# Kernel tuning notes

Hardware: AMD Instinct MI355X
Metric: run time of the kernel (lower is better)

Reference implementation:

```python
import jax, jax.numpy as jnp
import numpy as np

EPS = 1e-5

def _layernorm(x, gamma, beta):
    mu = jnp.mean(x, axis=-1, keepdims=True)
    var = jnp.var(x, axis=-1, keepdims=True)
    return (x - mu) * jax.lax.rsqrt(var + EPS) * gamma + beta

def setup_inputs() -> dict:
    key = jax.random.key(0)
    ks = jax.random.split(key, 6)
    bs, t, dim = 4, 2048, 1024
    x = jax.random.normal(ks[0], (bs, t, dim), dtype=jnp.float32)
    # shared LayerNorm params (same module applied twice in forward)
    ln_gamma = jnp.ones((dim,), dtype=jnp.float32)
    ln_beta = jnp.zeros((dim,), dtype=jnp.float32)
    # Linear params, stored as (in, out)
    w1 = jax.random.normal(ks[1], (dim, 2 * dim), dtype=jnp.float32) / np.sqrt(dim)
    b1 = jax.random.normal(ks[2], (2 * dim,), dtype=jnp.float32) * 0.01
    w2 = jax.random.normal(ks[3], (2 * dim, dim), dtype=jnp.float32) / np.sqrt(2 * dim)
    b2 = jax.random.normal(ks[4], (dim,), dtype=jnp.float32) * 0.01
    return {"x": x, "ln_gamma": ln_gamma, "ln_beta": ln_beta,
            "w1": w1, "b1": b1, "w2": w2, "b2": b2}

def reference(x, ln_gamma, ln_beta, w1, b1, w2, b2):
    # x: [bs, t, f]
    y = _layernorm(x, ln_gamma, ln_beta)
    y = jax.nn.gelu(jnp.einsum('btf,fh->bth', y, w1) + b1, approximate=False)
    y = jnp.einsum('bth,hf->btf', y, w2) + b2
    # attention-like quadratic mix (no softmax): (x @ x^T) @ y
    scores = jnp.einsum('btf,bsf->bts', x, x)          # [bs, t, t]
    y = jnp.einsum('bts,bsf->btf', scores, y)
    y = x + y
    y = _layernorm(y, ln_gamma, ln_beta)
    return y
```

## Files before the change

### kernel.cpp

```cpp
#include <hip/hip_runtime.h>
#include <hip/hip_fp16.h>

typedef _Float16 f16;
typedef _Float16 f16x8 __attribute__((ext_vector_type(8)));
typedef _Float16 f16x4 __attribute__((ext_vector_type(4)));
typedef float f32x4 __attribute__((ext_vector_type(4)));

#define LN_EPS 1e-5f

__device__ __forceinline__ float erf_fast(float x) {
    const float ax = __builtin_fabsf(x);
    const float t = 1.0f / (1.0f + 0.3275911f * ax);
    const float y = t * (0.254829592f +
                    t * (-0.284496736f +
                    t * (1.421413741f +
                    t * (-1.453152027f +
                    t * 1.061405429f))));
    const float r = 1.0f - y * __expf(-ax * ax);
    return __builtin_copysignf(r, x);
}

__device__ __forceinline__ float gelu_exact(float v) {
    return 0.5f * v * (1.0f + erf_fast(v * 0.70710678118654752440f));
}

__device__ __forceinline__ void gload_lds16(const f16* g, f16* l) {
    __builtin_amdgcn_global_load_lds(
        (const __attribute__((address_space(1))) unsigned int*)(g),
        (__attribute__((address_space(3))) unsigned int*)(l),
        16, 0, 0);
}

__global__ __launch_bounds__(256)
void ln_cast_kernel(const float* __restrict__ x,
                    const float* __restrict__ gamma,
                    const float* __restrict__ beta,
                    f16* __restrict__ y_h,
                    f16* __restrict__ x_h) {
    const int row = blockIdx.x;
    const int t = threadIdx.x;
    const size_t base = (size_t)row * 1024;
    float4 v = ((const float4*)(x + base))[t];
    float s  = v.x + v.y + v.z + v.w;
    float s2 = v.x*v.x + v.y*v.y + v.z*v.z + v.w*v.w;
    #pragma unroll
    for (int off = 32; off > 0; off >>= 1) {
        s  += __shfl_down(s, off, 64);
        s2 += __shfl_down(s2, off, 64);
    }
    __shared__ float ls[4], ls2[4];
    const int wid = t >> 6;
    if ((t & 63) == 0) { ls[wid] = s; ls2[wid] = s2; }
    __syncthreads();
    if (t == 0) {
        ls[0]  = ls[0] + ls[1] + ls[2] + ls[3];
        ls2[0] = ls2[0] + ls2[1] + ls2[2] + ls2[3];
    }
    __syncthreads();
    const float mu   = ls[0] * (1.0f / 1024.0f);
    const float var  = ls2[0] * (1.0f / 1024.0f) - mu * mu;
    const float rstd = rsqrtf(var + LN_EPS);
    const float4 g  = ((const float4*)gamma)[t];
    const float4 bt = ((const float4*)beta)[t];
    f16x4 yo, xo;
    yo[0] = (f16)((v.x - mu) * rstd * g.x + bt.x);
    yo[1] = (f16)((v.y - mu) * rstd * g.y + bt.y);
    yo[2] = (f16)((v.z - mu) * rstd * g.z + bt.z);
    yo[3] = (f16)((v.w - mu) * rstd * g.w + bt.w);
    xo[0] = (f16)v.x; xo[1] = (f16)v.y; xo[2] = (f16)v.z; xo[3] = (f16)v.w;
    *(f16x4*)(y_h + base + t * 4) = yo;
    *(f16x4*)(x_h + base + t * 4) = xo;
}

__global__ __launch_bounds__(256)
void ln_final_kernel(const float* __restrict__ pre,
                     const float* __restrict__ gamma,
                     const float* __restrict__ beta,
                     float* __restrict__ out) {
    const int row = blockIdx.x;
    const int t = threadIdx.x;
    const size_t base = (size_t)row * 1024;
    float4 v = ((const float4*)(pre + base))[t];
    float s  = v.x + v.y + v.z + v.w;
    float s2 = v.x*v.x + v.y*v.y + v.z*v.z + v.w*v.w;
    #pragma unroll
    for (int off = 32; off > 0; off >>= 1) {
        s  += __shfl_down(s, off, 64);
        s2 += __shfl_down(s2, off, 64);
    }
    __shared__ float ls[4], ls2[4];
    const int wid = t >> 6;
    if ((t & 63) == 0) { ls[wid] = s; ls2[wid] = s2; }
    __syncthreads();
    if (t == 0) {
        ls[0]  = ls[0] + ls[1] + ls[2] + ls[3];
        ls2[0] = ls2[0] + ls2[1] + ls2[2] + ls2[3];
    }
    __syncthreads();
    const float mu   = ls[0] * (1.0f / 1024.0f);
    const float var  = ls2[0] * (1.0f / 1024.0f) - mu * mu;
    const float rstd = rsqrtf(var + LN_EPS);
    const float4 g  = ((const float4*)gamma)[t];
    const float4 bt = ((const float4*)beta)[t];
    float4 o;
    o.x = (v.x - mu) * rstd * g.x + bt.x;
    o.y = (v.y - mu) * rstd * g.y + bt.y;
    o.z = (v.z - mu) * rstd * g.z + bt.z;
    o.w = (v.w - mu) * rstd * g.w + bt.w;
    ((float4*)(out + base))[t] = o;
}

__global__ __launch_bounds__(256)
void transpose_cast_kernel(const float* __restrict__ src,
                           f16* __restrict__ dst, int R, int C) {
    __shared__ float tile[32][33];
    const int c0 = blockIdx.x * 32, r0 = blockIdx.y * 32;
    const int tx = threadIdx.x & 31, ty = threadIdx.x >> 5;
    #pragma unroll
    for (int i = 0; i < 4; ++i) {
        const int r = ty + i * 8;
        tile[r][tx] = src[(size_t)(r0 + r) * C + c0 + tx];
    }
    __syncthreads();
    #pragma unroll
    for (int i = 0; i < 4; ++i) {
        const int r = ty + i * 8;
        dst[(size_t)(c0 + r) * R + r0 + tx] = (f16)tile[tx][r];
    }
}

__global__ __launch_bounds__(256)
void transpose_f16_kernel(const f16* __restrict__ src,
                          f16* __restrict__ dst, int R, int C) {
    __shared__ f16 tile[32][33];
    const size_t zb = (size_t)blockIdx.z * R * C;
    src += zb; dst += zb;
    const int c0 = blockIdx.x * 32, r0 = blockIdx.y * 32;
    const int tx = threadIdx.x & 31, ty = threadIdx.x >> 5;
    #pragma unroll
    for (int i = 0; i < 4; ++i) {
        const int r = ty + i * 8;
        tile[r][tx] = src[(size_t)(r0 + r) * C + c0 + tx];
    }
    __syncthreads();
    #pragma unroll
    for (int i = 0; i < 4; ++i) {
        const int r = ty + i * 8;
        dst[(size_t)(c0 + r) * R + r0 + tx] = tile[tx][r];
    }
}

template <int EPI>
__global__ __launch_bounds__(512, 2)
void gemm256_nt_kernel(const f16* __restrict__ A, const f16* __restrict__ Bt,
                       const float* __restrict__ bias, f16* __restrict__ outH,
                       int M, int N, int K) {
    __shared__ __attribute__((aligned(16))) f16 sAbuf[2][256 * 64];
    __shared__ __attribute__((aligned(16))) f16 sBbuf[2][256 * 64];

    const int m0 = blockIdx.x * 256;
    const int n0 = blockIdx.y * 256;
    const int t = threadIdx.x;
    const int l = t & 63;
    const int wid = t >> 6;
    const int wr = wid >> 2;
    const int wc = wid & 3;
    const int rl = l & 15;
    const int g  = l >> 4;
    const int nk = K >> 6;

    const int rowS = wid * 16 + (l >> 3);
    const int kbS  = ((l & 7) ^ ((l >> 3) & 7)) * 8;
    const f16* pA = A  + (size_t)(m0 + rowS) * K + kbS;
    const f16* pB = Bt + (size_t)(n0 + rowS) * K + kbS;
    const int ldsS = wid * 1024;

    const int rA = wr * 128 + rl;
    const int rB = wc * 64 + rl;
    const int swk0 = ((g)     ^ (rl & 7)) * 8;
    const int swk1 = ((4 + g) ^ (rl & 7)) * 8;

    f32x4 acc[8][4] = {};

    const long long hstep = (long long)128 * K;

    auto stgA = [&](f16* dst, int h, int kc) {
        const f16* s = pA + (size_t)h * hstep + kc * 64;
        f16* d = dst + h * 8192 + ldsS;
        gload_lds16(s, d);
        gload_lds16(s + 8 * K, d + 512);
    };
    auto stgB = [&](f16* dst, int h, int kc) {
        const f16* s = pB + (size_t)h * hstep + kc * 64;
        f16* d = dst + h * 8192 + ldsS;
        gload_lds16(s, d);
        gload_lds16(s + 8 * K, d + 512);
    };

    f16* bufA0 = sAbuf[0]; f16* bufA1 = sAbuf[1];
    f16* bufB0 = sBbuf[0]; f16* bufB1 = sBbuf[1];

    const int t1 = (nk > 1) ? 1 : 0;
    stgA(bufA0, 0, 0); stgA(bufA0, 1, 0);
    stgB(bufB0, 0, 0); stgB(bufB0, 1, 0);
    stgB(bufB1, 0, t1); stgB(bufB1, 1, t1);
    stgA(bufA1, 0, t1);
    asm volatile("s_waitcnt vmcnt(6)" ::: "memory");
    __builtin_amdgcn_s_barrier();

    f16 *Ac = bufA0, *Ao = bufA1, *Bc = bufB0, *Bo = bufB1;

    f16x8 a[4][2], b0r[2][2], b1r[2][2];

    for (int kt = 0; kt < nk; ++kt) {
        const int kt1 = (kt + 1 < nk) ? kt + 1 : nk - 1;
        const int kt2 = (kt + 2 < nk) ? kt + 2 : nk - 1;

        #pragma unroll
        for (int fm = 0; fm < 4; ++fm) {
            a[fm][0] = *(const f16x8*)(Ac + (rA + fm * 16) * 64 + swk0);
            a[fm][1] = *(const f16x8*)(Ac + (rA + fm * 16) * 64 + swk1);
        }
        #pragma unroll
        for (int fn = 0; fn < 2; ++fn) {
            b0r[fn][0] = *(const f16x8*)(Bc + (rB + fn * 16) * 64 + swk0);
            b0r[fn][1] = *(const f16x8*)(Bc + (rB + fn * 16) * 64 + swk1);
        }
        stgA(Ao, 1, kt1);
        __builtin_amdgcn_s_barrier();
        asm volatile("s_waitcnt lgkmcnt(0)" ::: "memory");
        __builtin_amdgcn_sched_barrier(0);
        __builtin_amdgcn_s_setprio(1);
        #pragma unroll
        for (int fm = 0; fm < 4; ++fm)
            #pragma unroll
            for (int fn = 0; fn < 2; ++fn) {
                acc[fm][fn] = __builtin_amdgcn_mfma_f32_16x16x32_f16(a[fm][0], b0r[fn][0], acc[fm][fn], 0, 0, 0);
                acc[fm][fn] = __builtin_amdgcn_mfma_f32_16x16x32_f16(a[fm][1], b0r[fn][1], acc[fm][fn], 0, 0, 0);
            }
        __builtin_amdgcn_s_setprio(0);
        __builtin_amdgcn_s_barrier();

        #pragma unroll
        for (int fn = 0; fn < 2; ++fn) {
            b1r[fn][0] = *(const f16x8*)(Bc + (rB + (fn + 2) * 16) * 64 + swk0);
            b1r[fn][1] = *(const f16x8*)(Bc + (rB + (fn + 2) * 16) * 64 + swk1);
        }
        __builtin_amdgcn_s_barrier();
        asm volatile("s_waitcnt lgkmcnt(0)" ::: "memory");
        __builtin_amdgcn_sched_barrier(0);
        __builtin_amdgcn_s_setprio(1);
        #pragma unroll
        for (int fm = 0; fm < 4; ++fm)
            #pragma unroll
            for (int fn = 0; fn < 2; ++fn) {
                acc[fm][fn + 2] = __builtin_amdgcn_mfma_f32_16x16x32_f16(a[fm][0], b1r[fn][0], acc[fm][fn + 2], 0, 0, 0);
                acc[fm][fn + 2] = __builtin_amdgcn_mfma_f32_16x16x32_f16(a[fm][1], b1r[fn][1], acc[fm][fn + 2], 0, 0, 0);
            }
        __builtin_amdgcn_s_setprio(0);
        __builtin_amdgcn_s_barrier();

        #pragma unroll
        for (int fm = 0; fm < 4; ++fm) {
            a[fm][0] = *(const f16x8*)(Ac + (rA + (fm + 4) * 16) * 64 + swk0);
            a[fm][1] = *(const f16x8*)(Ac + (rA + (fm + 4) * 16) * 64 + swk1);
        }
        stgB(Bc, 0, kt2);
        __builtin_amdgcn_s_barrier();
        asm volatile("s_waitcnt lgkmcnt(0)" ::: "memory");
        __builtin_amdgcn_sched_barrier(0);
        __builtin_amdgcn_s_setprio(1);
        #pragma unroll
        for (int fm = 0; fm < 4; ++fm)
            #pragma unroll
            for (int fn = 0; fn < 2; ++fn) {
                acc[fm + 4][fn + 2] = __builtin_amdgcn_mfma_f32_16x16x32_f16(a[fm][0], b1r[fn][0], acc[fm + 4][fn + 2], 0, 0, 0);
                acc[fm + 4][fn + 2] = __builtin_amdgcn_mfma_f32_16x16x32_f16(a[fm][1], b1r[fn][1], acc[fm + 4][fn + 2], 0, 0, 0);
            }
        __builtin_amdgcn_s_setprio(0);
        __builtin_amdgcn_s_barrier();

        stgB(Bc, 1, kt2);
        stgA(Ac, 0, kt2);
        __builtin_amdgcn_s_barrier();
        __builtin_amdgcn_s_setprio(1);
        #pragma unroll
        for (int fm = 0; fm < 4; ++fm)
            #pragma unroll
            for (int fn = 0; fn < 2; ++fn) {
                acc[fm + 4][fn] = __builtin_amdgcn_mfma_f32_16x16x32_f16(a[fm][0], b0r[fn][0], acc[fm + 4][fn], 0, 0, 0);
                acc[fm + 4][fn] = __builtin_amdgcn_mfma_f32_16x16x32_f16(a[fm][1], b0r[fn][1], acc[fm + 4][fn], 0, 0, 0);
            }
        __builtin_amdgcn_s_setprio(0);
        asm volatile("s_waitcnt vmcnt(6)" ::: "memory");
        __builtin_amdgcn_s_barrier();

        f16* tp;
        tp = Ac; Ac = Ao; Ao = tp;
        tp = Bc; Bc = Bo; Bo = tp;
    }
    asm volatile("s_waitcnt vmcnt(0)" ::: "memory");

    #pragma unroll
    for (int fm = 0; fm < 8; ++fm) {
        #pragma unroll
        for (int fn = 0; fn < 4; ++fn) {
            const int col = n0 + wc * 64 + fn * 16 + rl;
            const float bv = bias[col];
            #pragma unroll
            for (int r = 0; r < 4; ++r) {
                const int row = m0 + wr * 128 + fm * 16 + g * 4 + r;
                const float v = acc[fm][fn][r] + bv;
                outH[(size_t)row * N + col] = (f16)gelu_exact(v);
            }
        }
    }
}

template <int EPI>
__global__ __launch_bounds__(512, 2)
void gemm256x128_nt_kernel(const f16* __restrict__ A, const f16* __restrict__ Bt,
                           const float* __restrict__ bias,
                           const float* __restrict__ xadd,
                           f16* __restrict__ outH, float* __restrict__ outF,
                           int M, int N, int K,
                           long long batchA, long long batchB, long long batchC) {
    __shared__ __attribute__((aligned(16))) f16 sA[3][256 * 64];
    __shared__ __attribute__((aligned(16))) f16 sB[3][128 * 64];

    const int z = blockIdx.z;
    A  += (size_t)z * batchA;
    Bt += (size_t)z * batchB;

    const int m0 = blockIdx.x * 256;
    const int n0 = blockIdx.y * 128;
    const int t = threadIdx.x;
    const int l = t & 63;
    const int wid = t >> 6;
    const int wr = wid >> 1;
    const int wc = wid & 1;
    const int rl = l & 15;
    const int g  = l >> 4;
    const int nk = K >> 6;

    const int rowS = t >> 3;
    const int kbS  = ((t & 7) ^ (rowS & 7)) * 8;
    const f16* pA = A  + (size_t)(m0 + rowS) * K + kbS;
    const f16* pB = Bt + (size_t)(n0 + rowS) * K + kbS;
    const int ldsS = wid * 512;

    const int rA = wr * 64 + rl;
    const int rB = wc * 64 + rl;
    const int swk0 = ((g)     ^ (rl & 7)) * 8;
    const int swk1 = ((4 + g) ^ (rl & 7)) * 8;

    f32x4 acc[4][4] = {};

    auto stgA = [&](f16* dst, int u, int kc) {
        gload_lds16(pA + (size_t)u * 64 * K + kc * 64, dst + u * 4096 + ldsS);
    };
    auto stgB = [&](f16* dst, int u, int kc) {
        gload_lds16(pB + (size_t)u * 64 * K + kc * 64, dst + u * 4096 + ldsS);
    };

    const int t1 = (nk > 1) ? 1 : 0;
    #pragma unroll
    for (int u = 0; u < 4; ++u) stgA(sA[0], u, 0);
    #pragma unroll
    for (int u = 0; u < 2; ++u) stgB(sB[0], u, 0);
    #pragma unroll
    for (int u = 0; u < 4; ++u) stgA(sA[1], u, t1);
    #pragma unroll
    for (int u = 0; u < 2; ++u) stgB(sB[1], u, t1);

    f16 *curA = sA[0], *nxtA = sA[1], *farA = sA[2];
    f16 *curB = sB[0], *nxtB = sB[1], *farB = sB[2];

    f16x8 a[4][2], b[4][2];

    for (int kt = 0; kt < nk; ++kt) {
        asm volatile("s_waitcnt vmcnt(6)" ::: "memory");
        __builtin_amdgcn_s_barrier();

        const int kt2 = (kt + 2 < nk) ? kt + 2 : nk - 1;

        #pragma unroll
        for (int fm = 0; fm < 2; ++fm) {
            a[fm][0] = *(const f16x8*)(curA + (rA + fm * 16) * 64 + swk0);
            a[fm][1] = *(const f16x8*)(curA + (rA + fm * 16) * 64 + swk1);
        }
        #pragma unroll
        for (int fn = 0; fn < 2; ++fn) {
            b[fn][0] = *(const f16x8*)(curB + (rB + fn * 16) * 64 + swk0);
            b[fn][1] = *(const f16x8*)(curB + (rB + fn * 16) * 64 + swk1);
        }
        stgA(farA, 0, kt2);
        stgA(farA, 1, kt2);
        asm volatile("s_waitcnt lgkmcnt(0)" ::: "memory");
        __builtin_amdgcn_sched_barrier(0);
        __builtin_amdgcn_s_setprio(1);
        #pragma unroll
        for (int fm = 0; fm < 2; ++fm)
            #pragma unroll
            for (int fn = 0; fn < 2; ++fn) {
                acc[fm][fn] = __builtin_amdgcn_mfma_f32_16x16x32_f16(a[fm][0], b[fn][0], acc[fm][fn], 0, 0, 0);
                acc[fm][fn] = __builtin_amdgcn_mfma_f32_16x16x32_f16(a[fm][1], b[fn][1], acc[fm][fn], 0, 0, 0);
            }
        __builtin_amdgcn_s_setprio(0);

        #pragma unroll
        for (int fn = 2; fn < 4; ++fn) {
            b[fn][0] = *(const f16x8*)(curB + (rB + fn * 16) * 64 + swk0);
            b[fn][1] = *(const f16x8*)(curB + (rB + fn * 16) * 64 + swk1);
        }
        stgA(farA, 2, kt2);
        stgA(farA, 3, kt2);
        asm volatile("s_waitcnt lgkmcnt(0)" ::: "memory");
        __builtin_amdgcn_sched_barrier(0);
        __builtin_amdgcn_s_setprio(1);
        #pragma unroll
        for (int fm = 0; fm < 2; ++fm)
            #pragma unroll
            for (int fn = 2; fn < 4; ++fn) {
                acc[fm][fn] = __builtin_amdgcn_mfma_f32_16x16x32_f16(a[fm][0], b[fn][0], acc[fm][fn], 0, 0, 0);
                acc[fm][fn] = __builtin_amdgcn_mfma_f32_16x16x32_f16(a[fm][1], b[fn][1], acc[fm][fn], 0, 0, 0);
            }
        __builtin_amdgcn_s_setprio(0);

        #pragma unroll
        for (int fm = 2; fm < 4; ++fm) {
            a[fm][0] = *(const f16x8*)(curA + (rA + fm * 16) * 64 + swk0);
            a[fm][1] = *(const f16x8*)(curA + (rA + fm * 16) * 64 + swk1);
        }
        stgB(farB, 0, kt2);
        stgB(farB, 1, kt2);
        asm volatile("s_waitcnt lgkmcnt(0)" ::: "memory");
        __builtin_amdgcn_sched_barrier(0);
        __builtin_amdgcn_s_setprio(1);
        #pragma unroll
        for (int fm = 2; fm < 4; ++fm)
            #pragma unroll
            for (int fn = 2; fn < 4; ++fn) {
                acc[fm][fn] = __builtin_amdgcn_mfma_f32_16x16x32_f16(a[fm][0], b[fn][0], acc[fm][fn], 0, 0, 0);
                acc[fm][fn] = __builtin_amdgcn_mfma_f32_16x16x32_f16(a[fm][1], b[fn][1], acc[fm][fn], 0, 0, 0);
            }
        __builtin_amdgcn_s_setprio(0);

        __builtin_amdgcn_s_setprio(1);
        #pragma unroll
        for (int fm = 2; fm < 4; ++fm)
            #pragma unroll
            for (int fn = 0; fn < 2; ++fn) {
                acc[fm][fn] = __builtin_amdgcn_mfma_f32_16x16x32_f16(a[fm][0], b[fn][0], acc[fm][fn], 0, 0, 0);
                acc[fm][fn] = __builtin_amdgcn_mfma_f32_16x16x32_f16(a[fm][1], b[fn][1], acc[fm][fn], 0, 0, 0);
            }
        __builtin_amdgcn_s_setprio(0);

        f16* tp;
        tp = curA; curA = nxtA; nxtA = farA; farA = tp;
        tp = curB; curB = nxtB; nxtB = farB; farB = tp;
    }
    asm volatile("s_waitcnt vmcnt(0)" ::: "memory");

    const float* xaddz = xadd;
    float* outFz = outF;
    if (EPI == 3) {
        outFz += (size_t)z * batchC;
        xaddz += (size_t)z * batchC;
    }
    #pragma unroll
    for (int fm = 0; fm < 4; ++fm) {
        #pragma unroll
        for (int fn = 0; fn < 4; ++fn) {
            const int col = n0 + wc * 64 + fn * 16 + rl;
            if (EPI == 1) {
                const int row0 = m0 + wr * 64 + fm * 16 + g * 4;
                const int zz = row0 >> 11;
                const int rr = row0 & 2047;
                const float bv = bias[col];
                f16x4 o;
                #pragma unroll
                for (int r = 0; r < 4; ++r) o[r] = (f16)(acc[fm][fn][r] + bv);
                *(f16x4*)(outH + ((size_t)zz * N + col) * 2048 + rr) = o;
            } else {
                #pragma unroll
                for (int r = 0; r < 4; ++r) {
                    const int row = m0 + wr * 64 + fm * 16 + g * 4 + r;
                    const size_t idx = (size_t)row * N + col;
                    outFz[idx] = acc[fm][fn][r] + xaddz[idx];
                }
            }
        }
    }
}

template <int EPI>
__global__ __launch_bounds__(256, 3)
void gemm_nt_kernel(const f16* __restrict__ A, const f16* __restrict__ Bt,
                    f16* __restrict__ outH,
                    int M, int N, int K,
                    long long batchA, long long batchB, long long batchC) {
    __shared__ __attribute__((aligned(16))) f16 sA[3][128 * 32];
    __shared__ __attribute__((aligned(16))) f16 sB[3][128 * 32];

    const int z = blockIdx.z;
    A  += (size_t)z * batchA;
    Bt += (size_t)z * batchB;

    const int m0 = blockIdx.x * 128;
    const int n0 = blockIdx.y * 128;
    const int t = threadIdx.x;
    const int l = t & 63;
    const int wid = t >> 6;
    const int wm = (wid >> 1) * 64;
    const int wn = (wid & 1) * 64;

    f32x4 acc[4][4] = {};

    const int rl = l & 15;
    const int nk = K >> 5;

    const int row0 = t >> 2;
    const int kb = ((t & 3) ^ (row0 & 3)) * 8;
    const f16* Ag0 = A  + (size_t)(m0 + row0) * K + kb;
    const f16* Ag1 = A  + (size_t)(m0 + row0 + 64) * K + kb;
    const f16* Bg0 = Bt + (size_t)(n0 + row0) * K + kb;
    const f16* Bg1 = Bt + (size_t)(n0 + row0 + 64) * K + kb;
    const int lo0 = wid * 512;
    const int lo1 = 2048 + wid * 512;

    const int swk = (((l >> 4) ^ (rl & 3))) * 8;

    gload_lds16(Ag0,      sA[0] + lo0);
    gload_lds16(Ag1,      sA[0] + lo1);
    gload_lds16(Bg0,      sB[0] + lo0);
    gload_lds16(Bg1,      sB[0] + lo1);
    gload_lds16(Ag0 + 32, sA[1] + lo0);
    gload_lds16(Ag1 + 32, sA[1] + lo1);
    gload_lds16(Bg0 + 32, sB[1] + lo0);
    gload_lds16(Bg1 + 32, sB[1] + lo1);

    f16 *curA = sA[0], *nxtA = sA[1], *farA = sA[2];
    f16 *curB = sB[0], *nxtB = sB[1], *farB = sB[2];

    for (int kt = 0; kt < nk; ++kt) {
        asm volatile("s_waitcnt vmcnt(4)" ::: "memory");
        __builtin_amdgcn_s_barrier();

        const int ktn = (kt + 2 < nk) ? kt + 2 : nk - 1;
        const int kof = ktn * 32;
        gload_lds16(Ag0 + kof, farA + lo0);
        gload_lds16(Ag1 + kof, farA + lo1);
        gload_lds16(Bg0 + kof, farB + lo0);
        gload_lds16(Bg1 + kof, farB + lo1);

        f16x8 a[4], b[4];
        #pragma unroll
        for (int f = 0; f < 4; ++f) {
            a[f] = *(const f16x8*)&curA[(wm + f * 16 + rl) * 32 + swk];
            b[f] = *(const f16x8*)&curB[(wn + f * 16 + rl) * 32 + swk];
        }
        #pragma unroll
        for (int fm = 0; fm < 4; ++fm)
            #pragma unroll
            for (int fn = 0; fn < 4; ++fn)
                acc[fm][fn] = __builtin_amdgcn_mfma_f32_16x16x32_f16(
                    a[fm], b[fn], acc[fm][fn], 0, 0, 0);

        f16* tA = curA; curA = nxtA; nxtA = farA; farA = tA;
        f16* tB = curB; curB = nxtB; nxtB = farB; farB = tB;
    }
    asm volatile("s_waitcnt vmcnt(0)" ::: "memory");

    const int rh = l >> 4;
    f16* outHz = outH + (size_t)z * batchC;
    #pragma unroll
    for (int fm = 0; fm < 4; ++fm) {
        #pragma unroll
        for (int fn = 0; fn < 4; ++fn) {
            const int col = n0 + wn + fn * 16 + rl;
            #pragma unroll
            for (int r = 0; r < 4; ++r) {
                const int row = m0 + wm + fm * 16 + rh * 4 + r;
                outHz[(size_t)row * N + col] = (f16)acc[fm][fn][r];
            }
        }
    }
}

extern "C" void kernel_launch(void* const* d_in, const int* in_sizes, int n_in,
                              void* d_out, int out_size, void* d_ws, size_t ws_size,
                              hipStream_t stream) {
    const float* x     = (const float*)d_in[0];
    const float* gamma = (const float*)d_in[1];
    const float* beta  = (const float*)d_in[2];
    const float* w1    = (const float*)d_in[3];
    const float* b1    = (const float*)d_in[4];
    const float* w2    = (const float*)d_in[5];
    const float* b2    = (const float*)d_in[6];
    float* out = (float*)d_out;

    const int BS = 4, T = 2048, DIM = 1024, HID = 2048;
    const int M = BS * T;
    const long long MB = 1024 * 1024;

    char* ws = (char*)d_ws;
    f16*   x_h  = (f16*)(ws + 0 * MB);
    f16*   y_h  = (f16*)(ws + 16 * MB);
    f16*   h    = (f16*)(ws + 32 * MB);
    float* pre  = (float*)h;
    f16*   y2t  = (f16*)(ws + 64 * MB);
    f16*   x_t  = (f16*)(ws + 80 * MB);
    f16*   G    = (f16*)(ws + 96 * MB);
    f16*   w1t  = (f16*)(ws + 104 * MB);
    f16*   w2t  = (f16*)(ws + 108 * MB);

    ln_cast_kernel<<<M, 256, 0, stream>>>(x, gamma, beta, y_h, x_h);

    transpose_cast_kernel<<<dim3(HID / 32, DIM / 32), 256, 0, stream>>>(w1, w1t, DIM, HID);
    transpose_cast_kernel<<<dim3(DIM / 32, HID / 32), 256, 0, stream>>>(w2, w2t, HID, DIM);

    gemm256_nt_kernel<0><<<dim3(M / 256, HID / 256), 512, 0, stream>>>(
        y_h, w1t, b1, h, M, HID, DIM);

    gemm256x128_nt_kernel<1><<<dim3(M / 256, DIM / 128, 1), 512, 0, stream>>>(
        h, w2t, b2, nullptr, y2t, nullptr, M, DIM, HID, 0, 0, 0);

    transpose_f16_kernel<<<dim3(DIM / 32, T / 32, BS), 256, 0, stream>>>(x_h, x_t, T, DIM);

    gemm_nt_kernel<2><<<dim3(DIM / 128, DIM / 128, BS), 256, 0, stream>>>(
        y2t, x_t, G, DIM, DIM, T,
        (long long)DIM * T, (long long)DIM * T, (long long)DIM * DIM);

    gemm256x128_nt_kernel<3><<<dim3(T / 256, DIM / 128, BS), 512, 0, stream>>>(
        x_h, G, nullptr, x, nullptr, pre, T, DIM, DIM,
        (long long)T * DIM, (long long)DIM * DIM, (long long)T * DIM);

    ln_final_kernel<<<M, 256, 0, stream>>>(pre, gamma, beta, out);
}
```

Baseline: 198.4 us.

## Swap MFMA operands for row-contiguous vector stores; reuse 256x128 kernel for first GEMM

Swaps the A/B operands of the MFMA instructions in most GEMM epilogues, so each lane holds four consecutive columns of one row. This lets the epilogues write f16x4 or float4 vectors instead of scattered scalar stores, and read bias and the residual as float4. The 256x256 first-GEMM kernel is removed, and the first GEMM now runs on the 256x128 kernel with a GELU epilogue, doubling its grid. The trade is less operand reuse per block on that first GEMM in exchange for wider, coalesced stores.

```diff
diff --git a/kernel.cpp b/kernel.cpp
--- a/kernel.cpp
+++ b/kernel.cpp
@@ -152,173 +152,6 @@
 
 template <int EPI>
 __global__ __launch_bounds__(512, 2)
-void gemm256_nt_kernel(const f16* __restrict__ A, const f16* __restrict__ Bt,
-                       const float* __restrict__ bias, f16* __restrict__ outH,
-                       int M, int N, int K) {
-    __shared__ __attribute__((aligned(16))) f16 sAbuf[2][256 * 64];
-    __shared__ __attribute__((aligned(16))) f16 sBbuf[2][256 * 64];
-
-    const int m0 = blockIdx.x * 256;
-    const int n0 = blockIdx.y * 256;
-    const int t = threadIdx.x;
-    const int l = t & 63;
-    const int wid = t >> 6;
-    const int wr = wid >> 2;
-    const int wc = wid & 3;
-    const int rl = l & 15;
-    const int g  = l >> 4;
-    const int nk = K >> 6;
-
-    const int rowS = wid * 16 + (l >> 3);
-    const int kbS  = ((l & 7) ^ ((l >> 3) & 7)) * 8;
-    const f16* pA = A  + (size_t)(m0 + rowS) * K + kbS;
-    const f16* pB = Bt + (size_t)(n0 + rowS) * K + kbS;
-    const int ldsS = wid * 1024;
-
-    const int rA = wr * 128 + rl;
-    const int rB = wc * 64 + rl;
-    const int swk0 = ((g)     ^ (rl & 7)) * 8;
-    const int swk1 = ((4 + g) ^ (rl & 7)) * 8;
-
-    f32x4 acc[8][4] = {};
-
-    const long long hstep = (long long)128 * K;
-
-    auto stgA = [&](f16* dst, int h, int kc) {
-        const f16* s = pA + (size_t)h * hstep + kc * 64;
-        f16* d = dst + h * 8192 + ldsS;
-        gload_lds16(s, d);
-        gload_lds16(s + 8 * K, d + 512);
-    };
-    auto stgB = [&](f16* dst, int h, int kc) {
-        const f16* s = pB + (size_t)h * hstep + kc * 64;
-        f16* d = dst + h * 8192 + ldsS;
-        gload_lds16(s, d);
-        gload_lds16(s + 8 * K, d + 512);
-    };
-
-    f16* bufA0 = sAbuf[0]; f16* bufA1 = sAbuf[1];
-    f16* bufB0 = sBbuf[0]; f16* bufB1 = sBbuf[1];
-
-    const int t1 = (nk > 1) ? 1 : 0;
-    stgA(bufA0, 0, 0); stgA(bufA0, 1, 0);
-    stgB(bufB0, 0, 0); stgB(bufB0, 1, 0);
-    stgB(bufB1, 0, t1); stgB(bufB1, 1, t1);
-    stgA(bufA1, 0, t1);
-    asm volatile("s_waitcnt vmcnt(6)" ::: "memory");
-    __builtin_amdgcn_s_barrier();
-
-    f16 *Ac = bufA0, *Ao = bufA1, *Bc = bufB0, *Bo = bufB1;
-
-    f16x8 a[4][2], b0r[2][2], b1r[2][2];
-
-    for (int kt = 0; kt < nk; ++kt) {
-        const int kt1 = (kt + 1 < nk) ? kt + 1 : nk - 1;
-        const int kt2 = (kt + 2 < nk) ? kt + 2 : nk - 1;
-
-        #pragma unroll
-        for (int fm = 0; fm < 4; ++fm) {
-            a[fm][0] = *(const f16x8*)(Ac + (rA + fm * 16) * 64 + swk0);
-            a[fm][1] = *(const f16x8*)(Ac + (rA + fm * 16) * 64 + swk1);
-        }
-        #pragma unroll
-        for (int fn = 0; fn < 2; ++fn) {
-            b0r[fn][0] = *(const f16x8*)(Bc + (rB + fn * 16) * 64 + swk0);
-            b0r[fn][1] = *(const f16x8*)(Bc + (rB + fn * 16) * 64 + swk1);
-        }
-        stgA(Ao, 1, kt1);
-        __builtin_amdgcn_s_barrier();
-        asm volatile("s_waitcnt lgkmcnt(0)" ::: "memory");
-        __builtin_amdgcn_sched_barrier(0);
-        __builtin_amdgcn_s_setprio(1);
-        #pragma unroll
-        for (int fm = 0; fm < 4; ++fm)
-            #pragma unroll
-            for (int fn = 0; fn < 2; ++fn) {
-                acc[fm][fn] = __builtin_amdgcn_mfma_f32_16x16x32_f16(a[fm][0], b0r[fn][0], acc[fm][fn], 0, 0, 0);
-                acc[fm][fn] = __builtin_amdgcn_mfma_f32_16x16x32_f16(a[fm][1], b0r[fn][1], acc[fm][fn], 0, 0, 0);
-            }
-        __builtin_amdgcn_s_setprio(0);
-        __builtin_amdgcn_s_barrier();
-
-        #pragma unroll
-        for (int fn = 0; fn < 2; ++fn) {
-            b1r[fn][0] = *(const f16x8*)(Bc + (rB + (fn + 2) * 16) * 64 + swk0);
-            b1r[fn][1] = *(const f16x8*)(Bc + (rB + (fn + 2) * 16) * 64 + swk1);
-        }
-        __builtin_amdgcn_s_barrier();
-        asm volatile("s_waitcnt lgkmcnt(0)" ::: "memory");
-        __builtin_amdgcn_sched_barrier(0);
-        __builtin_amdgcn_s_setprio(1);
-        #pragma unroll
-        for (int fm = 0; fm < 4; ++fm)
-            #pragma unroll
-            for (int fn = 0; fn < 2; ++fn) {
-                acc[fm][fn + 2] = __builtin_amdgcn_mfma_f32_16x16x32_f16(a[fm][0], b1r[fn][0], acc[fm][fn + 2], 0, 0, 0);
-                acc[fm][fn + 2] = __builtin_amdgcn_mfma_f32_16x16x32_f16(a[fm][1], b1r[fn][1], acc[fm][fn + 2], 0, 0, 0);
-            }
-        __builtin_amdgcn_s_setprio(0);
-        __builtin_amdgcn_s_barrier();
-
-        #pragma unroll
-        for (int fm = 0; fm < 4; ++fm) {
-            a[fm][0] = *(const f16x8*)(Ac + (rA + (fm + 4) * 16) * 64 + swk0);
-            a[fm][1] = *(const f16x8*)(Ac + (rA + (fm + 4) * 16) * 64 + swk1);
-        }
-        stgB(Bc, 0, kt2);
-        __builtin_amdgcn_s_barrier();
-        asm volatile("s_waitcnt lgkmcnt(0)" ::: "memory");
-        __builtin_amdgcn_sched_barrier(0);
-        __builtin_amdgcn_s_setprio(1);
-        #pragma unroll
-        for (int fm = 0; fm < 4; ++fm)
-            #pragma unroll
-            for (int fn = 0; fn < 2; ++fn) {
-                acc[fm + 4][fn + 2] = __builtin_amdgcn_mfma_f32_16x16x32_f16(a[fm][0], b1r[fn][0], acc[fm + 4][fn + 2], 0, 0, 0);
-                acc[fm + 4][fn + 2] = __builtin_amdgcn_mfma_f32_16x16x32_f16(a[fm][1], b1r[fn][1], acc[fm + 4][fn + 2], 0, 0, 0);
-            }
-        __builtin_amdgcn_s_setprio(0);
-        __builtin_amdgcn_s_barrier();
-
-        stgB(Bc, 1, kt2);
-        stgA(Ac, 0, kt2);
-        __builtin_amdgcn_s_barrier();
-        __builtin_amdgcn_s_setprio(1);
-        #pragma unroll
-        for (int fm = 0; fm < 4; ++fm)
-            #pragma unroll
-            for (int fn = 0; fn < 2; ++fn) {
-                acc[fm + 4][fn] = __builtin_amdgcn_mfma_f32_16x16x32_f16(a[fm][0], b0r[fn][0], acc[fm + 4][fn], 0, 0, 0);
-                acc[fm + 4][fn] = __builtin_amdgcn_mfma_f32_16x16x32_f16(a[fm][1], b0r[fn][1], acc[fm + 4][fn], 0, 0, 0);
-            }
-        __builtin_amdgcn_s_setprio(0);
-        asm volatile("s_waitcnt vmcnt(6)" ::: "memory");
-        __builtin_amdgcn_s_barrier();
-
-        f16* tp;
-        tp = Ac; Ac = Ao; Ao = tp;
-        tp = Bc; Bc = Bo; Bo = tp;
-    }
-    asm volatile("s_waitcnt vmcnt(0)" ::: "memory");
-
-    #pragma unroll
-    for (int fm = 0; fm < 8; ++fm) {
-        #pragma unroll
-        for (int fn = 0; fn < 4; ++fn) {
-            const int col = n0 + wc * 64 + fn * 16 + rl;
-            const float bv = bias[col];
-            #pragma unroll
-            for (int r = 0; r < 4; ++r) {
-                const int row = m0 + wr * 128 + fm * 16 + g * 4 + r;
-                const float v = acc[fm][fn][r] + bv;
-                outH[(size_t)row * N + col] = (f16)gelu_exact(v);
-            }
-        }
-    }
-}
-
-template <int EPI>
-__global__ __launch_bounds__(512, 2)
 void gemm256x128_nt_kernel(const f16* __restrict__ A, const f16* __restrict__ Bt,
                            const float* __restrict__ bias,
                            const float* __restrict__ xadd,
@@ -356,6 +189,13 @@
 
     f32x4 acc[4][4] = {};
 
+    auto mf = [&](f32x4 c, f16x8 af, f16x8 bf) {
+        if constexpr (EPI != 1)
+            return __builtin_amdgcn_mfma_f32_16x16x32_f16(bf, af, c, 0, 0, 0);
+        else
+            return __builtin_amdgcn_mfma_f32_16x16x32_f16(af, bf, c, 0, 0, 0);
+    };
+
     auto stgA = [&](f16* dst, int u, int kc) {
         gload_lds16(pA + (size_t)u * 64 * K + kc * 64, dst + u * 4096 + ldsS);
     };
@@ -403,8 +243,8 @@
         for (int fm = 0; fm < 2; ++fm)
             #pragma unroll
             for (int fn = 0; fn < 2; ++fn) {
-                acc[fm][fn] = __builtin_amdgcn_mfma_f32_16x16x32_f16(a[fm][0], b[fn][0], acc[fm][fn], 0, 0, 0);
-                acc[fm][fn] = __builtin_amdgcn_mfma_f32_16x16x32_f16(a[fm][1], b[fn][1], acc[fm][fn], 0, 0, 0);
+                acc[fm][fn] = mf(acc[fm][fn], a[fm][0], b[fn][0]);
+                acc[fm][fn] = mf(acc[fm][fn], a[fm][1], b[fn][1]);
             }
         __builtin_amdgcn_s_setprio(0);
 
@@ -422,8 +262,8 @@
         for (int fm = 0; fm < 2; ++fm)
             #pragma unroll
             for (int fn = 2; fn < 4; ++fn) {
-                acc[fm][fn] = __builtin_amdgcn_mfma_f32_16x16x32_f16(a[fm][0], b[fn][0], acc[fm][fn], 0, 0, 0);
-                acc[fm][fn] = __builtin_amdgcn_mfma_f32_16x16x32_f16(a[fm][1], b[fn][1], acc[fm][fn], 0, 0, 0);
+                acc[fm][fn] = mf(acc[fm][fn], a[fm][0], b[fn][0]);
+                acc[fm][fn] = mf(acc[fm][fn], a[fm][1], b[fn][1]);
             }
         __builtin_amdgcn_s_setprio(0);
 
@@ -441,8 +281,8 @@
         for (int fm = 2; fm < 4; ++fm)
             #pragma unroll
             for (int fn = 2; fn < 4; ++fn) {
-                acc[fm][fn] = __builtin_amdgcn_mfma_f32_16x16x32_f16(a[fm][0], b[fn][0], acc[fm][fn], 0, 0, 0);
-                acc[fm][fn] = __builtin_amdgcn_mfma_f32_16x16x32_f16(a[fm][1], b[fn][1], acc[fm][fn], 0, 0, 0);
+                acc[fm][fn] = mf(acc[fm][fn], a[fm][0], b[fn][0]);
+                acc[fm][fn] = mf(acc[fm][fn], a[fm][1], b[fn][1]);
             }
         __builtin_amdgcn_s_setprio(0);
 
@@ -451,8 +291,8 @@
         for (int fm = 2; fm < 4; ++fm)
             #pragma unroll
             for (int fn = 0; fn < 2; ++fn) {
-                acc[fm][fn] = __builtin_amdgcn_mfma_f32_16x16x32_f16(a[fm][0], b[fn][0], acc[fm][fn], 0, 0, 0);
-                acc[fm][fn] = __builtin_amdgcn_mfma_f32_16x16x32_f16(a[fm][1], b[fn][1], acc[fm][fn], 0, 0, 0);
+                acc[fm][fn] = mf(acc[fm][fn], a[fm][0], b[fn][0]);
+                acc[fm][fn] = mf(acc[fm][fn], a[fm][1], b[fn][1]);
             }
         __builtin_amdgcn_s_setprio(0);
 
@@ -462,18 +302,12 @@
     }
     asm volatile("s_waitcnt vmcnt(0)" ::: "memory");
 
-    const float* xaddz = xadd;
-    float* outFz = outF;
-    if (EPI == 3) {
-        outFz += (size_t)z * batchC;
-        xaddz += (size_t)z * batchC;
-    }
-    #pragma unroll
-    for (int fm = 0; fm < 4; ++fm) {
-        #pragma unroll
-        for (int fn = 0; fn < 4; ++fn) {
-            const int col = n0 + wc * 64 + fn * 16 + rl;
-            if (EPI == 1) {
+    if (EPI == 1) {
+        #pragma unroll
+        for (int fm = 0; fm < 4; ++fm) {
+            #pragma unroll
+            for (int fn = 0; fn < 4; ++fn) {
+                const int col = n0 + wc * 64 + fn * 16 + rl;
                 const int row0 = m0 + wr * 64 + fm * 16 + g * 4;
                 const int zz = row0 >> 11;
                 const int rr = row0 & 2047;
@@ -482,19 +316,44 @@
                 #pragma unroll
                 for (int r = 0; r < 4; ++r) o[r] = (f16)(acc[fm][fn][r] + bv);
                 *(f16x4*)(outH + ((size_t)zz * N + col) * 2048 + rr) = o;
-            } else {
-                #pragma unroll
-                for (int r = 0; r < 4; ++r) {
-                    const int row = m0 + wr * 64 + fm * 16 + g * 4 + r;
-                    const size_t idx = (size_t)row * N + col;
-                    outFz[idx] = acc[fm][fn][r] + xaddz[idx];
+            }
+        }
+    } else {
+        const float* xaddz = xadd;
+        float* outFz = outF;
+        if (EPI == 3) {
+            outFz += (size_t)z * batchC;
+            xaddz += (size_t)z * batchC;
+        }
+        #pragma unroll
+        for (int fm = 0; fm < 4; ++fm) {
+            const int row = m0 + wr * 64 + fm * 16 + rl;
+            #pragma unroll
+            for (int fn = 0; fn < 4; ++fn) {
+                const int colb = n0 + wc * 64 + fn * 16 + g * 4;
+                if (EPI == 0) {
+                    const float4 bv = *(const float4*)&bias[colb];
+                    f16x4 o;
+                    o[0] = (f16)gelu_exact(acc[fm][fn][0] + bv.x);
+                    o[1] = (f16)gelu_exact(acc[fm][fn][1] + bv.y);
+                    o[2] = (f16)gelu_exact(acc[fm][fn][2] + bv.z);
+                    o[3] = (f16)gelu_exact(acc[fm][fn][3] + bv.w);
+                    *(f16x4*)(outH + (size_t)row * N + colb) = o;
+                } else {
+                    const size_t idx = (size_t)row * N + colb;
+                    const float4 xa = *(const float4*)&xaddz[idx];
+                    float4 o;
+                    o.x = acc[fm][fn][0] + xa.x;
+                    o.y = acc[fm][fn][1] + xa.y;
+                    o.z = acc[fm][fn][2] + xa.z;
+                    o.w = acc[fm][fn][3] + xa.w;
+                    *(float4*)(outFz + idx) = o;
                 }
             }
         }
     }
 }
 
-template <int EPI>
 __global__ __launch_bounds__(256, 3)
 void gemm_nt_kernel(const f16* __restrict__ A, const f16* __restrict__ Bt,
                     f16* __restrict__ outH,
@@ -565,7 +424,7 @@
             #pragma unroll
             for (int fn = 0; fn < 4; ++fn)
                 acc[fm][fn] = __builtin_amdgcn_mfma_f32_16x16x32_f16(
-                    a[fm], b[fn], acc[fm][fn], 0, 0, 0);
+                    b[fn], a[fm], acc[fm][fn], 0, 0, 0);
 
         f16* tA = curA; curA = nxtA; nxtA = farA; farA = tA;
         f16* tB = curB; curB = nxtB; nxtB = farB; farB = tB;
@@ -576,14 +435,14 @@
     f16* outHz = outH + (size_t)z * batchC;
     #pragma unroll
     for (int fm = 0; fm < 4; ++fm) {
+        const int row = m0 + wm + fm * 16 + rl;
         #pragma unroll
         for (int fn = 0; fn < 4; ++fn) {
-            const int col = n0 + wn + fn * 16 + rl;
-            #pragma unroll
-            for (int r = 0; r < 4; ++r) {
-                const int row = m0 + wm + fm * 16 + rh * 4 + r;
-                outHz[(size_t)row * N + col] = (f16)acc[fm][fn][r];
-            }
+            const int colb = n0 + wn + fn * 16 + rh * 4;
+            f16x4 o;
+            #pragma unroll
+            for (int r = 0; r < 4; ++r) o[r] = (f16)acc[fm][fn][r];
+            *(f16x4*)(outHz + (size_t)row * N + colb) = o;
         }
     }
 }
@@ -620,15 +479,15 @@
     transpose_cast_kernel<<<dim3(HID / 32, DIM / 32), 256, 0, stream>>>(w1, w1t, DIM, HID);
     transpose_cast_kernel<<<dim3(DIM / 32, HID / 32), 256, 0, stream>>>(w2, w2t, HID, DIM);
 
-    gemm256_nt_kernel<0><<<dim3(M / 256, HID / 256), 512, 0, stream>>>(
-        y_h, w1t, b1, h, M, HID, DIM);
+    gemm256x128_nt_kernel<0><<<dim3(M / 256, HID / 128, 1), 512, 0, stream>>>(
+        y_h, w1t, b1, nullptr, h, nullptr, M, HID, DIM, 0, 0, 0);
 
     gemm256x128_nt_kernel<1><<<dim3(M / 256, DIM / 128, 1), 512, 0, stream>>>(
         h, w2t, b2, nullptr, y2t, nullptr, M, DIM, HID, 0, 0, 0);
 
     transpose_f16_kernel<<<dim3(DIM / 32, T / 32, BS), 256, 0, stream>>>(x_h, x_t, T, DIM);
 
-    gemm_nt_kernel<2><<<dim3(DIM / 128, DIM / 128, BS), 256, 0, stream>>>(
+    gemm_nt_kernel<<<dim3(DIM / 128, DIM / 128, BS), 256, 0, stream>>>(
         y2t, x_t, G, DIM, DIM, T,
         (long long)DIM * T, (long long)DIM * T, (long long)DIM * DIM);
 
```

Result: no change. 202.1 us (+1.9%).
